# Kernel optimization log

Measured on AMD Instinct MI355X. Metric: run time of the kernel, lower is better.

The kernel has to match this reference:

```python
import jax, jax.numpy as jnp
import numpy as np

N = 100000   # nodes
E = 1600000  # edges (avg degree 16)
D = 128      # input = hidden = out dim
L = 4        # num_layers
EPS = 1e-5   # LayerNorm eps


def setup_inputs() -> dict:
    key = jax.random.key(0)
    k0, k1, k2, k3, k4 = jax.random.split(key, 5)
    in_feat = jax.random.normal(k0, (N, D), dtype=jnp.float32)
    edge_index = jax.random.randint(k1, (2, E), 0, N, dtype=jnp.int32)
    s = 1.0 / np.sqrt(D)
    # GraphConv params per layer: lin_rel (weight+bias), lin_root (weight, no bias)
    W_rel = jax.random.uniform(k2, (L, D, D), jnp.float32, -s, s)
    b_rel = jax.random.uniform(k3, (L, D), jnp.float32, -s, s)
    W_root = jax.random.uniform(k4, (L, D, D), jnp.float32, -s, s)
    # single shared LayerNorm module in the torch code
    ln_gamma = jnp.ones((D,), jnp.float32)
    ln_beta = jnp.zeros((D,), jnp.float32)
    return {"in_feat": in_feat, "edge_index": edge_index, "W_rel": W_rel,
            "b_rel": b_rel, "W_root": W_root, "ln_gamma": ln_gamma, "ln_beta": ln_beta}


def _layer_norm(h, gamma, beta):
    mu = jnp.mean(h, axis=-1, keepdims=True)
    var = jnp.mean(jnp.square(h - mu), axis=-1, keepdims=True)
    return (h - mu) * jax.lax.rsqrt(var + EPS) * gamma + beta


def _graph_conv(h, W_r, b_r, W_rt, src, dst):
    # PyG GraphConv: out_i = lin_rel(sum_{j->i} x_j) + lin_root(x_i)
    agg = jax.ops.segment_sum(h[src], dst, num_segments=N)  # [N, D]
    return agg @ W_r + b_r + h @ W_rt


def reference(in_feat, edge_index, W_rel, b_rel, W_root, ln_gamma, ln_beta):
    src, dst = edge_index[0], edge_index[1]
    # input layer: conv -> ReLU -> LayerNorm -> dropout(p=0)
    h = _graph_conv(in_feat, W_rel[0], b_rel[0], W_root[0], src, dst)
    h = _layer_norm(jax.nn.relu(h), ln_gamma, ln_beta)
    # middle layers with residual
    for l in range(1, L - 1):
        nh = _graph_conv(h, W_rel[l], b_rel[l], W_root[l], src, dst)
        h = _layer_norm(jax.nn.relu(nh + h), ln_gamma, ln_beta)
    # output layer: conv only
    return _graph_conv(h, W_rel[L - 1], b_rel[L - 1], W_root[L - 1], src, dst)
```

## Files before the change

### kernel.cpp

```cpp
#include <hip/hip_runtime.h>
#include <cstddef>

#define N_NODES 100000
#define N_PAD   100032
#define N_EDGES 1600000
#define DIM 128
#define LN_EPS 1e-5f
#define ZROW   N_NODES
#define COL_CAP 3200000

#define B_SHIFT 9
#define B_SIZE  512
#define N_BKT   196
#define EPB     4096
#define NBLK    ((N_EDGES + EPB - 1) / EPB)

typedef short bf16x8 __attribute__((ext_vector_type(8)));
typedef float f32x4 __attribute__((ext_vector_type(4)));
typedef float f32x2 __attribute__((ext_vector_type(2)));

__device__ __forceinline__ float asf(uint u) {
    union { uint i; float f; } c; c.i = u; return c.f;
}
__device__ __forceinline__ float bf2f(uint u) { return asf(u << 16); }
__device__ __forceinline__ ushort f2bf(float x) {
    union { float f; uint i; } c; c.f = x;
    uint r = c.i + 0x7fffu + ((c.i >> 16) & 1u);
    return (ushort)(r >> 16);
}

__device__ __forceinline__ void accp(f32x2* acc, uint p) {
    f32x2 v;
    v.x = asf(p << 16);
    v.y = asf(p & 0xffff0000u);
    *acc += v;
}
__device__ __forceinline__ void accq(f32x2* a, uint4 p) {
    accp(&a[0], p.x); accp(&a[1], p.y); accp(&a[2], p.z); accp(&a[3], p.w);
}


__global__ __launch_bounds__(256) void bhist_kernel(const int* __restrict__ dst,
                                                    int* __restrict__ bcount) {
    __shared__ int lh[N_BKT];
    const int tid = threadIdx.x;
    if (tid < N_BKT) lh[tid] = 0;
    __syncthreads();
    const int base = blockIdx.x * EPB;
    #pragma unroll
    for (int k = 0; k < 16; ++k) {
        int t = base + tid + k * 256;
        if (t < N_EDGES) atomicAdd(&lh[dst[t] >> B_SHIFT], 1);
    }
    __syncthreads();
    if (tid < N_BKT && lh[tid]) atomicAdd(&bcount[tid], lh[tid]);
}

__global__ __launch_bounds__(256) void bscan_kernel(const int* __restrict__ bcount,
                                                    int* __restrict__ bstart,
                                                    int* __restrict__ gcur) {
    __shared__ int s[256];
    const int tid = threadIdx.x;
    int v = (tid < N_BKT) ? bcount[tid] : 0;
    s[tid] = v;
    __syncthreads();
    for (int off = 1; off < 256; off <<= 1) {
        int t = (tid >= off) ? s[tid - off] : 0;
        __syncthreads();
        s[tid] += t;
        __syncthreads();
    }
    if (tid < N_BKT) { int e = s[tid] - v; bstart[tid] = e; gcur[tid] = e; }
    if (tid == 0) bstart[N_BKT] = N_EDGES;
}

__global__ __launch_bounds__(256) void bscatter_kernel(const int* __restrict__ src,
                                                       const int* __restrict__ dst,
                                                       int* __restrict__ gcur,
                                                       int2* __restrict__ pairs) {
    __shared__ int lcnt[N_BKT];
    __shared__ int lbase[N_BKT];
    const int tid = threadIdx.x;
    if (tid < N_BKT) lcnt[tid] = 0;
    __syncthreads();
    const int base = blockIdx.x * EPB;
    int ls[16], ld[16];
    #pragma unroll
    for (int k = 0; k < 16; ++k) {
        int t = base + tid + k * 256;
        if (t < N_EDGES) {
            ls[k] = src[t]; ld[k] = dst[t];
            atomicAdd(&lcnt[ld[k] >> B_SHIFT], 1);
        } else ld[k] = -1;
    }
    __syncthreads();
    if (tid < N_BKT) lbase[tid] = lcnt[tid] ? atomicAdd(&gcur[tid], lcnt[tid]) : 0;
    __syncthreads();
    if (tid < N_BKT) lcnt[tid] = 0;
    __syncthreads();
    #pragma unroll
    for (int k = 0; k < 16; ++k) {
        if (ld[k] >= 0) {
            int b = ld[k] >> B_SHIFT;
            int r = atomicAdd(&lcnt[b], 1);
            pairs[lbase[b] + r] = make_int2(ls[k], ld[k]);
        }
    }
}

__global__ __launch_bounds__(256) void ndeg_kernel(const int2* __restrict__ pairs,
                                                   const int* __restrict__ bstart,
                                                   int* __restrict__ row_ptr,
                                                   int* __restrict__ bpad) {
    __shared__ int ldeg[B_SIZE];
    __shared__ int ws4[4];
    const int b = blockIdx.x;
    const int node0 = b << B_SHIFT;
    const int tid = threadIdx.x;
    ldeg[tid] = 0; ldeg[tid + 256] = 0;
    __syncthreads();
    const int beg = bstart[b], end = bstart[b + 1];
    for (int t = beg + tid; t < end; t += 256)
        atomicAdd(&ldeg[pairs[t].y - node0], 1);
    __syncthreads();
    const int d0 = (ldeg[2 * tid] + 15) & ~15;
    const int d1 = (ldeg[2 * tid + 1] + 15) & ~15;
    const int sum2 = d0 + d1;
    const int lane = tid & 63, wv = tid >> 6;
    int incl = sum2;
    #pragma unroll
    for (int off = 1; off < 64; off <<= 1) {
        int t = __shfl_up(incl, off);
        if (lane >= off) incl += t;
    }
    if (lane == 63) ws4[wv] = incl;
    __syncthreads();
    int woff = 0;
    if (wv > 0) woff += ws4[0];
    if (wv > 1) woff += ws4[1];
    if (wv > 2) woff += ws4[2];
    const int e0 = woff + incl - sum2;
    const int n0 = node0 + 2 * tid;
    if (n0 < N_NODES)     row_ptr[n0]     = e0;
    if (n0 + 1 < N_NODES) row_ptr[n0 + 1] = e0 + d0;
    if (tid == 255) bpad[b] = woff + incl;
}

__global__ __launch_bounds__(256) void pscan_kernel(const int* __restrict__ bpad,
                                                    int* __restrict__ bpadstart) {
    __shared__ int s[256];
    const int tid = threadIdx.x;
    int v = (tid < N_BKT) ? bpad[tid] : 0;
    s[tid] = v;
    __syncthreads();
    for (int off = 1; off < 256; off <<= 1) {
        int t = (tid >= off) ? s[tid - off] : 0;
        __syncthreads();
        s[tid] += t;
        __syncthreads();
    }
    if (tid < N_BKT) bpadstart[tid] = s[tid] - v;
    if (tid == N_BKT - 1) bpadstart[N_BKT] = s[tid];
}

__global__ void addbase_kernel(int* __restrict__ row_ptr, const int* __restrict__ bpadstart) {
    int n = blockIdx.x * 256 + threadIdx.x;
    if (n < N_NODES) row_ptr[n] += bpadstart[n >> B_SHIFT];
    if (n == N_NODES) row_ptr[N_NODES] = bpadstart[N_BKT];
}

__global__ void zfill_kernel(int4* __restrict__ col4) {
    int i = blockIdx.x * 256 + threadIdx.x;
    col4[i] = make_int4(ZROW, ZROW, ZROW, ZROW);
}

__global__ __launch_bounds__(256) void bfill_kernel(const int2* __restrict__ pairs,
                                                    const int* __restrict__ bstart,
                                                    const int* __restrict__ row_ptr,
                                                    int* __restrict__ col) {
    __shared__ int lcur[B_SIZE];
    const int b = blockIdx.x;
    const int node0 = b << B_SHIFT;
    const int tid = threadIdx.x;
    #pragma unroll
    for (int k = 0; k < 2; ++k) {
        int n = node0 + tid + k * 256;
        lcur[tid + k * 256] = (n < N_NODES) ? row_ptr[n] : 0;
    }
    __syncthreads();
    const int beg = bstart[b], end = bstart[b + 1];
    for (int t = beg + tid; t < end; t += 256) {
        int2 p = pairs[t];
        int r = atomicAdd(&lcur[p.y - node0], 1);
        col[r] = p.x;
    }
}


__global__ void cvt_kernel(const float* __restrict__ in, ushort* __restrict__ out) {
    int i = (blockIdx.x * blockDim.x + threadIdx.x) * 4;
    float4 v = *(const float4*)&in[i];
    uint2 r;
    r.x = (uint)f2bf(v.x) | ((uint)f2bf(v.y) << 16);
    r.y = (uint)f2bf(v.z) | ((uint)f2bf(v.w) << 16);
    *(uint2*)&out[i] = r;
}


__global__ void prepack_kernel(const float* __restrict__ Wrel, const float* __restrict__ Wroot,
                               ushort* __restrict__ Wp) {
    int t = blockIdx.x * blockDim.x + threadIdx.x;
    int layer = t >> 12;
    int tl = t & 4095;
    int frag = tl >> 6;
    int lane = tl & 63;
    int ks = frag >> 3, n = frag & 7;
    int c = n * 16 + (lane & 15);
    int k0 = ks * 32 + (lane >> 4) * 8;
    ushort tmp[8];
    #pragma unroll
    for (int j = 0; j < 8; ++j) {
        int kg = k0 + j;
        float w = (kg < 128) ? Wrel[layer * 16384 + kg * 128 + c]
                             : Wroot[layer * 16384 + (kg - 128) * 128 + c];
        tmp[j] = f2bf(w);
    }
    *(uint4*)&Wp[(size_t)t * 8] = *(const uint4*)tmp;
}


__global__ __launch_bounds__(256) void pull_kernel(const uint4* __restrict__ h,
                                                   const int* __restrict__ row_ptr,
                                                   const int* __restrict__ col,
                                                   uint4* __restrict__ agg, int npairs) {
    const int wid = threadIdx.x >> 6;
    const int lane = threadIdx.x & 63;
    const int pr = blockIdx.x * 4 + wid;
    if (pr >= npairs) return;
    const int nA = pr * 2, nB = nA + 1;
    const int rsel = lane >> 4;
    const int c16 = lane & 15;
    int jA = row_ptr[nA] + rsel;
    int jB = row_ptr[nB] + rsel;
    const int itA = (row_ptr[nA + 1] - (jA - rsel)) >> 4;
    const int itB = (row_ptr[nB + 1] - (jB - rsel)) >> 4;
    const int iters = max(itA, itB);

    f32x2 a[4], b[4];
    #pragma unroll
    for (int u = 0; u < 4; ++u) { a[u] = (f32x2){0.f, 0.f}; b[u] = (f32x2){0.f, 0.f}; }

    for (int it = 0; it < iters; ++it) {
        int sA0 = ZROW, sA1 = ZROW, sA2 = ZROW, sA3 = ZROW;
        int sB0 = ZROW, sB1 = ZROW, sB2 = ZROW, sB3 = ZROW;
        if (it < itA) {
            sA0 = col[jA]; sA1 = col[jA + 4]; sA2 = col[jA + 8]; sA3 = col[jA + 12];
            jA += 16;
        }
        if (it < itB) {
            sB0 = col[jB]; sB1 = col[jB + 4]; sB2 = col[jB + 8]; sB3 = col[jB + 12];
            jB += 16;
        }
        uint4 pA0 = h[(size_t)sA0 * 16 + c16];
        uint4 pA1 = h[(size_t)sA1 * 16 + c16];
        uint4 pA2 = h[(size_t)sA2 * 16 + c16];
        uint4 pA3 = h[(size_t)sA3 * 16 + c16];
        uint4 pB0 = h[(size_t)sB0 * 16 + c16];
        uint4 pB1 = h[(size_t)sB1 * 16 + c16];
        uint4 pB2 = h[(size_t)sB2 * 16 + c16];
        uint4 pB3 = h[(size_t)sB3 * 16 + c16];
        accq(a, pA0); accq(a, pA1); accq(a, pA2); accq(a, pA3);
        accq(b, pB0); accq(b, pB1); accq(b, pB2); accq(b, pB3);
    }

    #pragma unroll
    for (int u = 0; u < 4; ++u) {
        float ax = a[u].x, ay = a[u].y, bx = b[u].x, by = b[u].y;
        ax += __shfl_xor(ax, 16); ay += __shfl_xor(ay, 16);
        bx += __shfl_xor(bx, 16); by += __shfl_xor(by, 16);
        ax += __shfl_xor(ax, 32); ay += __shfl_xor(ay, 32);
        bx += __shfl_xor(bx, 32); by += __shfl_xor(by, 32);
        a[u].x = ax; a[u].y = ay; b[u].x = bx; b[u].y = by;
    }
    if (rsel == 0) {
        uint4 o;
        o.x = (uint)f2bf(a[0].x) | ((uint)f2bf(a[0].y) << 16);
        o.y = (uint)f2bf(a[1].x) | ((uint)f2bf(a[1].y) << 16);
        o.z = (uint)f2bf(a[2].x) | ((uint)f2bf(a[2].y) << 16);
        o.w = (uint)f2bf(a[3].x) | ((uint)f2bf(a[3].y) << 16);
        agg[(size_t)nA * 16 + c16] = o;
    } else if (rsel == 1) {
        uint4 o;
        o.x = (uint)f2bf(b[0].x) | ((uint)f2bf(b[0].y) << 16);
        o.y = (uint)f2bf(b[1].x) | ((uint)f2bf(b[1].y) << 16);
        o.z = (uint)f2bf(b[2].x) | ((uint)f2bf(b[2].y) << 16);
        o.w = (uint)f2bf(b[3].x) | ((uint)f2bf(b[3].y) << 16);
        agg[(size_t)nB * 16 + c16] = o;
    }
}


template <int MODE>
__global__ __launch_bounds__(256) void gemm_kernel(const ushort* __restrict__ aggb,
                                                   const ushort* __restrict__ hb,
                                                   const ushort* __restrict__ Wp,
                                                   const float* __restrict__ brel,
                                                   const float* __restrict__ gamma,
                                                   const float* __restrict__ beta,
                                                   ushort* __restrict__ outb,
                                                   float* __restrict__ outf) {
    __shared__ char sX[64 * 512];
    const int tid = threadIdx.x;
    const int row0 = blockIdx.x * 64;

    for (int c = tid; c < 2048; c += 256) {
        int r = c >> 5, cb = c & 31;
        const ushort* srcp = (cb < 16) ? &aggb[(size_t)(row0 + r) * 128 + cb * 8]
                                       : &hb[(size_t)(row0 + r) * 128 + (cb - 16) * 8];
        uint4 v = *(const uint4*)srcp;
        *(uint4*)&sX[r * 512 + ((cb * 16) ^ ((r & 7) << 4))] = v;
    }
    __syncthreads();

    const int lane = tid & 63;
    const int wv = tid >> 6;
    const int kg = lane >> 4;
    const int cl = lane & 15;
    const int ra = wv * 16 + cl;
    const int abase = ra * 512 + kg * 16;
    const int aswz = (ra & 7) << 4;

    f32x4 acc[8];
    #pragma unroll
    for (int n = 0; n < 8; ++n) acc[n] = (f32x4){0.f, 0.f, 0.f, 0.f};

    const uint4* bp = (const uint4*)Wp + lane;
    #pragma unroll 2
    for (int ks = 0; ks < 8; ++ks) {
        bf16x8 a = *(const bf16x8*)&sX[(abase + ks * 64) ^ aswz];
        #pragma unroll
        for (int n = 0; n < 8; ++n) {
            bf16x8 b = *(const bf16x8*)&bp[(ks * 8 + n) * 64];
            acc[n] = __builtin_amdgcn_mfma_f32_16x16x32_bf16(a, b, acc[n], 0, 0, 0);
        }
    }

    float bias[8], gg[8], bb[8];
    #pragma unroll
    for (int n = 0; n < 8; ++n) {
        int cn = n * 16 + cl;
        bias[n] = brel[cn];
        if (MODE != 2) { gg[n] = gamma[cn]; bb[n] = beta[cn]; }
    }

    #pragma unroll
    for (int reg = 0; reg < 4; ++reg) {
        const int r = wv * 16 + kg * 4 + reg;
        const size_t grow = (size_t)row0 + r;
        const bool live = grow < N_NODES;
        float v[8];
        float s = 0.f, q = 0.f;
        #pragma unroll
        for (int n = 0; n < 8; ++n) {
            float x = acc[n][reg] + bias[n];
            if (MODE == 1) {
                int cn = n * 16 + cl;
                ushort hu = *(const ushort*)&sX[r * 512 + ((256 + 2 * cn) ^ ((r & 7) << 4))];
                x += bf2f(hu);
            }
            if (MODE != 2) x = fmaxf(x, 0.f);
            v[n] = x; s += x; q += x * x;
        }
        if (MODE != 2) {
            #pragma unroll
            for (int m = 8; m >= 1; m >>= 1) { s += __shfl_xor(s, m); q += __shfl_xor(q, m); }
            float mu = s * (1.f / DIM);
            float var = q * (1.f / DIM) - mu * mu;
            float rinv = rsqrtf(var + LN_EPS);
            if (live) {
                #pragma unroll
                for (int n = 0; n < 8; ++n) {
                    float y = (v[n] - mu) * rinv * gg[n] + bb[n];
                    outb[grow * DIM + n * 16 + cl] = f2bf(y);
                }
            }
        } else {
            if (live) {
                #pragma unroll
                for (int n = 0; n < 8; ++n) outf[grow * DIM + n * 16 + cl] = v[n];
            }
        }
    }
}


static inline size_t align256(size_t x) { return (x + 255) & ~(size_t)255; }

extern "C" void kernel_launch(void* const* d_in, const int* in_sizes, int n_in,
                              void* d_out, int out_size, void* d_ws, size_t ws_size,
                              hipStream_t stream) {
    const float* in_feat = (const float*)d_in[0];
    const int*   ei      = (const int*)d_in[1];
    const float* Wrel    = (const float*)d_in[2];
    const float* brel    = (const float*)d_in[3];
    const float* Wroot   = (const float*)d_in[4];
    const float* gamma   = (const float*)d_in[5];
    const float* beta    = (const float*)d_in[6];
    float* out = (float*)d_out;

    char* ws = (char*)d_ws;
    size_t off = 0;
    int* col = (int*)(ws + off);        off = align256(off + (size_t)COL_CAP * 4);
    int2* pairs = (int2*)(ws + off);    off = align256(off + (size_t)N_EDGES * 8);
    int* row_ptr = (int*)(ws + off);    off = align256(off + (size_t)(N_NODES + 1) * 4);
    int* bcount = (int*)(ws + off);     off = align256(off + (size_t)N_BKT * 4);
    int* bstart = (int*)(ws + off);     off = align256(off + (size_t)(N_BKT + 1) * 4);
    int* gcur = (int*)(ws + off);       off = align256(off + (size_t)N_BKT * 4);
    int* bpad = (int*)(ws + off);       off = align256(off + (size_t)N_BKT * 4);
    int* bpadstart = (int*)(ws + off);  off = align256(off + (size_t)(N_BKT + 1) * 4);
    ushort* x0 = (ushort*)(ws + off);   off = align256(off + (size_t)N_PAD * DIM * 2);
    ushort* hA = (ushort*)(ws + off);   off = align256(off + (size_t)N_PAD * DIM * 2);
    ushort* hB = (ushort*)(ws + off);   off = align256(off + (size_t)N_PAD * DIM * 2);
    ushort* agg = (ushort*)(ws + off);  off = align256(off + (size_t)N_PAD * DIM * 2);
    ushort* Wp = (ushort*)(ws + off);   off = align256(off + (size_t)4 * 256 * 128 * 2);
    (void)ws_size; (void)in_sizes; (void)n_in; (void)out_size;

    const int* src = ei;
    const int* dst = ei + N_EDGES;

    hipMemsetAsync(bcount, 0, (size_t)N_BKT * 4, stream);
    bhist_kernel<<<NBLK, 256, 0, stream>>>(dst, bcount);
    bscan_kernel<<<1, 256, 0, stream>>>(bcount, bstart, gcur);
    bscatter_kernel<<<NBLK, 256, 0, stream>>>(src, dst, gcur, pairs);
    ndeg_kernel<<<N_BKT, 256, 0, stream>>>(pairs, bstart, row_ptr, bpad);
    pscan_kernel<<<1, 256, 0, stream>>>(bpad, bpadstart);
    addbase_kernel<<<(N_NODES + 256) / 256, 256, 0, stream>>>(row_ptr, bpadstart);
    zfill_kernel<<<COL_CAP / 1024, 256, 0, stream>>>((int4*)col);
    bfill_kernel<<<N_BKT, 256, 0, stream>>>(pairs, bstart, row_ptr, col);

    const size_t padoff = (size_t)N_NODES * DIM * 2;
    const size_t padlen = (size_t)(N_PAD - N_NODES) * DIM * 2;
    hipMemsetAsync((char*)x0 + padoff, 0, padlen, stream);
    hipMemsetAsync((char*)hA + padoff, 0, padlen, stream);
    hipMemsetAsync((char*)hB + padoff, 0, padlen, stream);
    hipMemsetAsync((char*)agg + padoff, 0, padlen, stream);

    cvt_kernel<<<(N_NODES * DIM) / (4 * 256), 256, 0, stream>>>(in_feat, x0);
    prepack_kernel<<<64, 256, 0, stream>>>(Wrel, Wroot, Wp);

    const int npairs = N_NODES / 2;
    const int pull_grid = (npairs + 3) / 4;
    const int gemm_grid = N_PAD / 64;

    pull_kernel<<<pull_grid, 256, 0, stream>>>((const uint4*)x0, row_ptr, col, (uint4*)agg, npairs);
    gemm_kernel<0><<<gemm_grid, 256, 0, stream>>>(agg, x0, Wp, brel, gamma, beta, hA, nullptr);
    pull_kernel<<<pull_grid, 256, 0, stream>>>((const uint4*)hA, row_ptr, col, (uint4*)agg, npairs);
    gemm_kernel<1><<<gemm_grid, 256, 0, stream>>>(agg, hA, Wp + 32768, brel + DIM, gamma, beta, hB, nullptr);
    pull_kernel<<<pull_grid, 256, 0, stream>>>((const uint4*)hB, row_ptr, col, (uint4*)agg, npairs);
    gemm_kernel<1><<<gemm_grid, 256, 0, stream>>>(agg, hB, Wp + 2 * 32768, brel + 2 * DIM, gamma, beta, hA, nullptr);
    pull_kernel<<<pull_grid, 256, 0, stream>>>((const uint4*)hA, row_ptr, col, (uint4*)agg, npairs);
    gemm_kernel<2><<<gemm_grid, 256, 0, stream>>>(agg, hA, Wp + 3 * 32768, brel + 3 * DIM, gamma, beta, nullptr, out);
}
```

Before: 440.3 us.

## Fuse neighbor aggregation into GEMM kernel, gathering directly into shared memory

Merges the pull (gather-sum) kernel and the GEMM kernel into one per-layer kernel. Each block aggregates neighbor rows for its 64 nodes straight into the shared-memory A tile, so the intermediate agg buffer and its global write/read round trip disappear, along with four kernel launches. The gather is now one node per wave per step (16 nodes sequentially per wave) instead of two interleaved nodes, which lowers memory-level parallelism in the latency-bound gather and could hurt. row_ptr is extended over the padded rows so the padding nodes see zero degree.

```diff
diff --git a/kernel.cpp b/kernel.cpp
--- a/kernel.cpp
+++ b/kernel.cpp
@@ -166,7 +166,7 @@
 __global__ void addbase_kernel(int* __restrict__ row_ptr, const int* __restrict__ bpadstart) {
     int n = blockIdx.x * 256 + threadIdx.x;
     if (n < N_NODES) row_ptr[n] += bpadstart[n >> B_SHIFT];
-    if (n == N_NODES) row_ptr[N_NODES] = bpadstart[N_BKT];
+    else if (n <= N_PAD) row_ptr[n] = bpadstart[N_BKT];
 }
 
 __global__ void zfill_kernel(int4* __restrict__ col4) {
@@ -229,101 +229,66 @@
 }
 
 
-__global__ __launch_bounds__(256) void pull_kernel(const uint4* __restrict__ h,
-                                                   const int* __restrict__ row_ptr,
-                                                   const int* __restrict__ col,
-                                                   uint4* __restrict__ agg, int npairs) {
-    const int wid = threadIdx.x >> 6;
-    const int lane = threadIdx.x & 63;
-    const int pr = blockIdx.x * 4 + wid;
-    if (pr >= npairs) return;
-    const int nA = pr * 2, nB = nA + 1;
+template <int MODE>
+__global__ __launch_bounds__(256) void fused_kernel(const ushort* __restrict__ hb,
+                                                    const int* __restrict__ row_ptr,
+                                                    const int* __restrict__ col,
+                                                    const ushort* __restrict__ Wp,
+                                                    const float* __restrict__ brel,
+                                                    const float* __restrict__ gamma,
+                                                    const float* __restrict__ beta,
+                                                    ushort* __restrict__ outb,
+                                                    float* __restrict__ outf) {
+    __shared__ char sX[64 * 512];
+    const int tid = threadIdx.x;
+    const int row0 = blockIdx.x * 64;
+    const int lane = tid & 63;
+    const int wv = tid >> 6;
     const int rsel = lane >> 4;
     const int c16 = lane & 15;
-    int jA = row_ptr[nA] + rsel;
-    int jB = row_ptr[nB] + rsel;
-    const int itA = (row_ptr[nA + 1] - (jA - rsel)) >> 4;
-    const int itB = (row_ptr[nB + 1] - (jB - rsel)) >> 4;
-    const int iters = max(itA, itB);
-
-    f32x2 a[4], b[4];
-    #pragma unroll
-    for (int u = 0; u < 4; ++u) { a[u] = (f32x2){0.f, 0.f}; b[u] = (f32x2){0.f, 0.f}; }
-
-    for (int it = 0; it < iters; ++it) {
-        int sA0 = ZROW, sA1 = ZROW, sA2 = ZROW, sA3 = ZROW;
-        int sB0 = ZROW, sB1 = ZROW, sB2 = ZROW, sB3 = ZROW;
-        if (it < itA) {
-            sA0 = col[jA]; sA1 = col[jA + 4]; sA2 = col[jA + 8]; sA3 = col[jA + 12];
-            jA += 16;
-        }
-        if (it < itB) {
-            sB0 = col[jB]; sB1 = col[jB + 4]; sB2 = col[jB + 8]; sB3 = col[jB + 12];
-            jB += 16;
-        }
-        uint4 pA0 = h[(size_t)sA0 * 16 + c16];
-        uint4 pA1 = h[(size_t)sA1 * 16 + c16];
-        uint4 pA2 = h[(size_t)sA2 * 16 + c16];
-        uint4 pA3 = h[(size_t)sA3 * 16 + c16];
-        uint4 pB0 = h[(size_t)sB0 * 16 + c16];
-        uint4 pB1 = h[(size_t)sB1 * 16 + c16];
-        uint4 pB2 = h[(size_t)sB2 * 16 + c16];
-        uint4 pB3 = h[(size_t)sB3 * 16 + c16];
-        accq(a, pA0); accq(a, pA1); accq(a, pA2); accq(a, pA3);
-        accq(b, pB0); accq(b, pB1); accq(b, pB2); accq(b, pB3);
-    }
-
-    #pragma unroll
-    for (int u = 0; u < 4; ++u) {
-        float ax = a[u].x, ay = a[u].y, bx = b[u].x, by = b[u].y;
-        ax += __shfl_xor(ax, 16); ay += __shfl_xor(ay, 16);
-        bx += __shfl_xor(bx, 16); by += __shfl_xor(by, 16);
-        ax += __shfl_xor(ax, 32); ay += __shfl_xor(ay, 32);
-        bx += __shfl_xor(bx, 32); by += __shfl_xor(by, 32);
-        a[u].x = ax; a[u].y = ay; b[u].x = bx; b[u].y = by;
-    }
-    if (rsel == 0) {
-        uint4 o;
-        o.x = (uint)f2bf(a[0].x) | ((uint)f2bf(a[0].y) << 16);
-        o.y = (uint)f2bf(a[1].x) | ((uint)f2bf(a[1].y) << 16);
-        o.z = (uint)f2bf(a[2].x) | ((uint)f2bf(a[2].y) << 16);
-        o.w = (uint)f2bf(a[3].x) | ((uint)f2bf(a[3].y) << 16);
-        agg[(size_t)nA * 16 + c16] = o;
-    } else if (rsel == 1) {
-        uint4 o;
-        o.x = (uint)f2bf(b[0].x) | ((uint)f2bf(b[0].y) << 16);
-        o.y = (uint)f2bf(b[1].x) | ((uint)f2bf(b[1].y) << 16);
-        o.z = (uint)f2bf(b[2].x) | ((uint)f2bf(b[2].y) << 16);
-        o.w = (uint)f2bf(b[3].x) | ((uint)f2bf(b[3].y) << 16);
-        agg[(size_t)nB * 16 + c16] = o;
-    }
-}
-
-
-template <int MODE>
-__global__ __launch_bounds__(256) void gemm_kernel(const ushort* __restrict__ aggb,
-                                                   const ushort* __restrict__ hb,
-                                                   const ushort* __restrict__ Wp,
-                                                   const float* __restrict__ brel,
-                                                   const float* __restrict__ gamma,
-                                                   const float* __restrict__ beta,
-                                                   ushort* __restrict__ outb,
-                                                   float* __restrict__ outf) {
-    __shared__ char sX[64 * 512];
-    const int tid = threadIdx.x;
-    const int row0 = blockIdx.x * 64;
-
-    for (int c = tid; c < 2048; c += 256) {
-        int r = c >> 5, cb = c & 31;
-        const ushort* srcp = (cb < 16) ? &aggb[(size_t)(row0 + r) * 128 + cb * 8]
-                                       : &hb[(size_t)(row0 + r) * 128 + (cb - 16) * 8];
-        uint4 v = *(const uint4*)srcp;
-        *(uint4*)&sX[r * 512 + ((cb * 16) ^ ((r & 7) << 4))] = v;
-    }
-    __syncthreads();
-
-    const int lane = tid & 63;
-    const int wv = tid >> 6;
+
+    for (int c = tid; c < 1024; c += 256) {
+        int r = c >> 4, cb = c & 15;
+        uint4 v = *(const uint4*)&hb[(size_t)(row0 + r) * 128 + cb * 8];
+        *(uint4*)&sX[r * 512 + ((256 + cb * 16) ^ ((r & 7) << 4))] = v;
+    }
+
+    const uint4* h4 = (const uint4*)hb;
+    for (int t = 0; t < 16; ++t) {
+        const int r = wv * 16 + t;
+        const int jbeg = row_ptr[row0 + r];
+        const int iters = (row_ptr[row0 + r + 1] - jbeg) >> 4;
+        f32x2 a[4];
+        #pragma unroll
+        for (int u = 0; u < 4; ++u) a[u] = (f32x2){0.f, 0.f};
+        int j = jbeg + rsel;
+        for (int it = 0; it < iters; ++it) {
+            int s0 = col[j], s1 = col[j + 4], s2 = col[j + 8], s3 = col[j + 12];
+            j += 16;
+            uint4 p0 = h4[(size_t)s0 * 16 + c16];
+            uint4 p1 = h4[(size_t)s1 * 16 + c16];
+            uint4 p2 = h4[(size_t)s2 * 16 + c16];
+            uint4 p3 = h4[(size_t)s3 * 16 + c16];
+            accq(a, p0); accq(a, p1); accq(a, p2); accq(a, p3);
+        }
+        #pragma unroll
+        for (int u = 0; u < 4; ++u) {
+            float ax = a[u].x, ay = a[u].y;
+            ax += __shfl_xor(ax, 16); ay += __shfl_xor(ay, 16);
+            ax += __shfl_xor(ax, 32); ay += __shfl_xor(ay, 32);
+            a[u].x = ax; a[u].y = ay;
+        }
+        if (rsel == 0) {
+            uint4 o;
+            o.x = (uint)f2bf(a[0].x) | ((uint)f2bf(a[0].y) << 16);
+            o.y = (uint)f2bf(a[1].x) | ((uint)f2bf(a[1].y) << 16);
+            o.z = (uint)f2bf(a[2].x) | ((uint)f2bf(a[2].y) << 16);
+            o.w = (uint)f2bf(a[3].x) | ((uint)f2bf(a[3].y) << 16);
+            *(uint4*)&sX[r * 512 + ((c16 * 16) ^ ((r & 7) << 4))] = o;
+        }
+    }
+    __syncthreads();
+
     const int kg = lane >> 4;
     const int cl = lane & 15;
     const int ra = wv * 16 + cl;
@@ -412,7 +377,7 @@
     size_t off = 0;
     int* col = (int*)(ws + off);        off = align256(off + (size_t)COL_CAP * 4);
     int2* pairs = (int2*)(ws + off);    off = align256(off + (size_t)N_EDGES * 8);
-    int* row_ptr = (int*)(ws + off);    off = align256(off + (size_t)(N_NODES + 1) * 4);
+    int* row_ptr = (int*)(ws + off);    off = align256(off + (size_t)(N_PAD + 2) * 4);
     int* bcount = (int*)(ws + off);     off = align256(off + (size_t)N_BKT * 4);
     int* bstart = (int*)(ws + off);     off = align256(off + (size_t)(N_BKT + 1) * 4);
     int* gcur = (int*)(ws + off);       off = align256(off + (size_t)N_BKT * 4);
@@ -421,7 +386,6 @@
     ushort* x0 = (ushort*)(ws + off);   off = align256(off + (size_t)N_PAD * DIM * 2);
     ushort* hA = (ushort*)(ws + off);   off = align256(off + (size_t)N_PAD * DIM * 2);
     ushort* hB = (ushort*)(ws + off);   off = align256(off + (size_t)N_PAD * DIM * 2);
-    ushort* agg = (ushort*)(ws + off);  off = align256(off + (size_t)N_PAD * DIM * 2);
     ushort* Wp = (ushort*)(ws + off);   off = align256(off + (size_t)4 * 256 * 128 * 2);
     (void)ws_size; (void)in_sizes; (void)n_in; (void)out_size;
 
@@ -434,7 +398,7 @@
     bscatter_kernel<<<NBLK, 256, 0, stream>>>(src, dst, gcur, pairs);
     ndeg_kernel<<<N_BKT, 256, 0, stream>>>(pairs, bstart, row_ptr, bpad);
     pscan_kernel<<<1, 256, 0, stream>>>(bpad, bpadstart);
-    addbase_kernel<<<(N_NODES + 256) / 256, 256, 0, stream>>>(row_ptr, bpadstart);
+    addbase_kernel<<<(N_PAD + 1 + 255) / 256, 256, 0, stream>>>(row_ptr, bpadstart);
     zfill_kernel<<<COL_CAP / 1024, 256, 0, stream>>>((int4*)col);
     bfill_kernel<<<N_BKT, 256, 0, stream>>>(pairs, bstart, row_ptr, col);
 
@@ -443,21 +407,14 @@
     hipMemsetAsync((char*)x0 + padoff, 0, padlen, stream);
     hipMemsetAsync((char*)hA + padoff, 0, padlen, stream);
     hipMemsetAsync((char*)hB + padoff, 0, padlen, stream);
-    hipMemsetAsync((char*)agg + padoff, 0, padlen, stream);
 
     cvt_kernel<<<(N_NODES * DIM) / (4 * 256), 256, 0, stream>>>(in_feat, x0);
     prepack_kernel<<<64, 256, 0, stream>>>(Wrel, Wroot, Wp);
 
-    const int npairs = N_NODES / 2;
-    const int pull_grid = (npairs + 3) / 4;
-    const int gemm_grid = N_PAD / 64;
-
-    pull_kernel<<<pull_grid, 256, 0, stream>>>((const uint4*)x0, row_ptr, col, (uint4*)agg, npairs);
-    gemm_kernel<0><<<gemm_grid, 256, 0, stream>>>(agg, x0, Wp, brel, gamma, beta, hA, nullptr);
-    pull_kernel<<<pull_grid, 256, 0, stream>>>((const uint4*)hA, row_ptr, col, (uint4*)agg, npairs);
-    gemm_kernel<1><<<gemm_grid, 256, 0, stream>>>(agg, hA, Wp + 32768, brel + DIM, gamma, beta, hB, nullptr);
-    pull_kernel<<<pull_grid, 256, 0, stream>>>((const uint4*)hB, row_ptr, col, (uint4*)agg, npairs);
-    gemm_kernel<1><<<gemm_grid, 256, 0, stream>>>(agg, hB, Wp + 2 * 32768, brel + 2 * DIM, gamma, beta, hA, nullptr);
-    pull_kernel<<<pull_grid, 256, 0, stream>>>((const uint4*)hA, row_ptr, col, (uint4*)agg, npairs);
-    gemm_kernel<2><<<gemm_grid, 256, 0, stream>>>(agg, hA, Wp + 3 * 32768, brel + 3 * DIM, gamma, beta, nullptr, out);
-}
+    const int grid = N_PAD / 64;
+
+    fused_kernel<0><<<grid, 256, 0, stream>>>(x0, row_ptr, col, Wp, brel, gamma, beta, hA, nullptr);
+    fused_kernel<1><<<grid, 256, 0, stream>>>(hA, row_ptr, col, Wp + 32768, brel + DIM, gamma, beta, hB, nullptr);
+    fused_kernel<1><<<grid, 256, 0, stream>>>(hB, row_ptr, col, Wp + 2 * 32768, brel + 2 * DIM, gamma, beta, hA, nullptr);
+    fused_kernel<2><<<grid, 256, 0, stream>>>(hA, row_ptr, col, Wp + 3 * 32768, brel + 3 * DIM, gamma, beta, nullptr, out);
+}
```

After: 447.7 us. Within noise of the previous version (+1.7%).
